# Kernel tuning notes

Measured on AMD Instinct MI355X. Metric: run time of the kernel, lower is better.

The kernel has to match this reference:

```python
import jax, jax.numpy as jnp
import numpy as np

NEG_SLOPE = 0.01  # torch F.leaky_relu default

def _lrelu(x):
    return jax.nn.leaky_relu(x, NEG_SLOPE)

def setup_inputs() -> dict:
    key = jax.random.key(0)
    ks = jax.random.split(key, 24)
    B, N, E = 512, 20000, 640000
    n_enc_1, n_enc_2, n_z = 512, 256, 64
    n_dec_2, n_dec_1, hidden = 256, 512, 256
    p = lambda k, shp, fan: jax.random.normal(k, shp, jnp.float32) * (1.0 / np.sqrt(fan))
    return {
        "data": jax.random.normal(ks[0], (B, N), jnp.float32),
        "noise": jax.random.normal(ks[1], (B, N), jnp.float32),
        "edge_index": jax.random.randint(ks[2], (2, E), 0, N, jnp.int32),
        "w_gcn": jax.random.normal(ks[3], (), jnp.float32),
        "b_gcn": jax.random.normal(ks[4], (), jnp.float32) * 0.1,
        "enc1_w": p(ks[5], (N, n_enc_1), N), "enc1_b": p(ks[6], (n_enc_1,), N),
        "enc2_w": p(ks[7], (n_enc_1, n_enc_2), n_enc_1), "enc2_b": p(ks[8], (n_enc_2,), n_enc_1),
        "enc3_w": p(ks[9], (n_enc_2, n_z), n_enc_2), "enc3_b": p(ks[10], (n_z,), n_enc_2),
        "dec1_w": p(ks[11], (n_z, n_dec_2), n_z), "dec1_b": p(ks[12], (n_dec_2,), n_z),
        "dec2_w": p(ks[13], (n_dec_2, n_dec_1), n_dec_2), "dec2_b": p(ks[14], (n_dec_1,), n_dec_2),
        "dec3_w": p(ks[15], (n_dec_1, N), n_dec_1), "dec3_b": p(ks[16], (N,), n_dec_1),
        "disc1_w": p(ks[17], (n_z, hidden), n_z), "disc1_b": p(ks[18], (hidden,), n_z),
        "disc2_w": p(ks[19], (hidden, hidden), hidden), "disc2_b": p(ks[20], (hidden,), hidden),
        "disc3_w": p(ks[21], (hidden, 1), hidden), "disc3_b": p(ks[22], (1,), hidden),
    }

def _gcn_batched(x, edge_index, w_gcn, b_gcn):
    # x: [B, N] -> GCNConv(1,1, improved=True) applied per row, vectorized.
    B, N = x.shape
    src, dst = edge_index[0], edge_index[1]
    loop = jnp.arange(N, dtype=src.dtype)
    src_a = jnp.concatenate([src, loop])
    dst_a = jnp.concatenate([dst, loop])
    # improved=True: self-loop edge weight 2.0
    ew = jnp.concatenate([jnp.ones(src.shape[0], x.dtype), jnp.full((N,), 2.0, x.dtype)])
    deg = jax.ops.segment_sum(ew, dst_a, num_segments=N)
    dinv = jnp.where(deg > 0, jax.lax.rsqrt(deg), 0.0)
    norm = dinv[src_a] * ew * dinv[dst_a]  # [E+N]
    xl = x * w_gcn                         # lin (1x1 weight, no bias)
    msgs = xl[:, src_a] * norm[None, :]    # [B, E+N]
    agg = jnp.zeros_like(x).at[:, dst_a].add(msgs)
    return agg + b_gcn

def reference(data, noise, edge_index, w_gcn, b_gcn,
              enc1_w, enc1_b, enc2_w, enc2_b, enc3_w, enc3_b,
              dec1_w, dec1_b, dec2_w, dec2_b, dec3_w, dec3_b,
              disc1_w, disc1_b, disc2_w, disc2_b, disc3_w, disc3_b):
    x = data + noise * 0.1
    gcn_out = _lrelu(_gcn_batched(x, edge_index, w_gcn, b_gcn))  # [B, N]
    h1 = _lrelu(gcn_out @ enc1_w + enc1_b)
    h2 = _lrelu(h1 @ enc2_w + enc2_b)
    z = _lrelu(h2 @ enc3_w + enc3_b)
    d1 = _lrelu(z @ dec1_w + dec1_b)
    d2 = _lrelu(d1 @ dec2_w + dec2_b)
    dec_h3 = _lrelu(d2 @ dec3_w + dec3_b)
    g1 = _lrelu(z @ disc1_w + disc1_b)
    g2 = _lrelu(g1 @ disc2_w + disc2_b)
    d = jax.nn.sigmoid(g2 @ disc3_w + disc3_b)
    return (dec_h3, z, d)
```

## Files before the change

### kernel.cpp

```cpp
#include <hip/hip_runtime.h>
#include <hip/hip_bf16.h>


#define LRELU(v) ((v) > 0.f ? (v) : 0.01f * (v))

static constexpr int Bb = 512;
static constexpr int Nn = 20000;
static constexpr int Ee = 640000;
static constexpr int KPAD = 20480;

typedef __attribute__((ext_vector_type(8))) short short8;
typedef __attribute__((ext_vector_type(4))) float f32x4;

__device__ __forceinline__ ushort f2bf(float f) {
  uint u = __builtin_bit_cast(uint, f);
  u = u + 0x7FFFu + ((u >> 16) & 1u);
  return (ushort)(u >> 16);
}
__device__ __forceinline__ float bfLo(uint u) {
  return __builtin_bit_cast(float, u << 16);
}
__device__ __forceinline__ float bfHi(uint u) {
  return __builtin_bit_cast(float, u & 0xffff0000u);
}

__global__ void transpose_xs_k(const float* __restrict__ a, const float* __restrict__ nz,
                               const float* __restrict__ dinv, ushort* __restrict__ xs, int b0) {
  __shared__ ushort tile[64][65];
  int c0 = blockIdx.x * 64;
  int p = blockIdx.y;
  int chunk = p >> 1;
  int sub = (p & 1) * 64;
  int rbase = b0 + p * 64;
  for (int i = threadIdx.x; i < 64 * 64; i += 256) {
    int rr = i >> 6, cc = i & 63;
    int r = rbase + rr, c = c0 + cc;
    ushort v = 0;
    if (c < Nn) {
      size_t idx = (size_t)r * Nn + c;
      v = f2bf(dinv[c] * (a[idx] + 0.1f * nz[idx]));
    }
    tile[rr][cc] = v;
  }
  __syncthreads();
  for (int i = threadIdx.x; i < 64 * 64; i += 256) {
    int cc = i >> 6, rr = i & 63;
    int c = c0 + cc;
    if (c < Nn) xs[(size_t)chunk * Nn * 128 + (size_t)c * 128 + sub + rr] = tile[rr][cc];
  }
}

__global__ void hist_check_k(const int* __restrict__ src, const int* __restrict__ dst, int E,
                             int* __restrict__ cnt, int* __restrict__ flag) {
  int i = blockIdx.x * 256 + threadIdx.x;
  if (i < E) {
    int s = src[i], d = dst[i];
    if ((unsigned)s >= (unsigned)Nn || (unsigned)d >= (unsigned)Nn) {
      atomicExch(flag, 1);
    } else {
      atomicAdd(&cnt[d], 1);
    }
  }
}

__global__ void offs_k(const int* __restrict__ cnt, int* __restrict__ offs,
                       int* __restrict__ cursor, float* __restrict__ dinv,
                       int* __restrict__ bump) {
  int i = blockIdx.x * 256 + threadIdx.x;
  int l = threadIdx.x & 63;
  int v = (i < Nn) ? cnt[i] : 0;
  int x = v;
#pragma unroll
  for (int d = 1; d < 64; d <<= 1) {
    int t = __shfl_up(x, d);
    if (l >= d) x += t;
  }
  int total = __shfl(x, 63);
  int base = 0;
  if (l == 0) base = atomicAdd(bump, total);
  base = __shfl(base, 0);
  int excl = base + x - v;
  if (i < Nn) {
    offs[i] = excl;
    cursor[i] = excl;
    dinv[i] = rsqrtf(2.0f + (float)v);
  }
}

__global__ void scatter_k(const int* __restrict__ src, const int* __restrict__ dst, int E,
                          int* __restrict__ cursor, uint* __restrict__ eOff) {
  int i = blockIdx.x * 256 + threadIdx.x;
  if (i < E) {
    int s = src[i], d = dst[i];
    if ((unsigned)s >= (unsigned)Nn || (unsigned)d >= (unsigned)Nn) return;
    int p = atomicAdd(&cursor[d], 1);
    eOff[p] = (uint)s * 256u;
  }
}

__global__ __launch_bounds__(256) void spmm_chunk_k(
    const ushort* __restrict__ xs, const uint* __restrict__ eOff, const int* __restrict__ offs,
    const int* __restrict__ cnt, const float* __restrict__ dinv, const float* __restrict__ wg,
    const float* __restrict__ bg, ushort* __restrict__ gcnT, int NC) {
  __shared__ uint sIdx[4][64];
  int bid = blockIdx.x;
  int chunk = bid % NC;
  int ngrp = bid / NC;
  int wv = threadIdx.x >> 6, l = threadIdx.x & 63;
  int n = ngrp * 4 + wv;
  int o = offs[n], c = cnt[n];
  const char* base = (const char*)(xs + (size_t)chunk * Nn * 128) + l * 4;
  const uint* ep = eOff + o;
  uint su = *(const uint*)(base + (size_t)n * 256);
  float a00 = 2.0f * bfLo(su), a01 = 2.0f * bfHi(su);
  float a10 = 0.f, a11 = 0.f;

  for (int bi = 0; bi < c; bi += 64) {
    int rem = c - bi;
    if (rem > 64) rem = 64;
    sIdx[wv][l] = (l < rem) ? ep[bi + l] : 0u;
    int i = 0;
    for (; i + 8 <= rem; i += 8) {
      uint u[8];
#pragma unroll
      for (int j = 0; j < 8; ++j) u[j] = *(const uint*)(base + sIdx[wv][i + j]);
#pragma unroll
      for (int j = 0; j < 8; j += 2) {
        a00 += bfLo(u[j]);
        a01 += bfHi(u[j]);
        a10 += bfLo(u[j + 1]);
        a11 += bfHi(u[j + 1]);
      }
    }
    for (; i < rem; ++i) {
      uint u = *(const uint*)(base + sIdx[wv][i]);
      a00 += bfLo(u);
      a01 += bfHi(u);
    }
  }

  float wdn = wg[0] * dinv[n], bb = bg[0];
  float v0 = wdn * (a00 + a10) + bb;
  float v1 = wdn * (a01 + a11) + bb;
  v0 = LRELU(v0);
  v1 = LRELU(v1);
  uint pk = (uint)f2bf(v0) | ((uint)f2bf(v1) << 16);
  *(uint*)&gcnT[(size_t)chunk * KPAD * 128 + (size_t)n * 128 + 2 * l] = pk;
}

template <bool SPLITK>
__global__ __launch_bounds__(256) void mfma_gemm(const ushort* __restrict__ AT, int lda, int pw,
                                                 size_t pstride, const float* __restrict__ B,
                                                 int ldb, int KB, int Nv, int iters,
                                                 float* __restrict__ C, int ldc,
                                                 const float* __restrict__ bias) {
  __shared__ ushort As[32 * 72];
  __shared__ ushort Bs[32 * 72];
  int n0 = blockIdx.x * 64, m0 = blockIdx.y * 64;
  int k0 = blockIdx.z * iters * 32;
  int tid = threadIdx.x;
  int skk = tid >> 3, sx0 = (tid & 7) * 8;
  int l = tid & 63, w = tid >> 6;
  int wr = w >> 1, wc = w & 1;
  int lrow = l & 15, lk8 = (l >> 4) * 8;
  const ushort* Ap = AT + (size_t)(m0 / pw) * pstride + (m0 % pw);
  f32x4 acc[2][2] = {};

  for (int kt = 0; kt < iters; ++kt) {
    int kg = k0 + kt * 32 + skk;
    uint4 av = *(const uint4*)&Ap[(size_t)kg * lda + sx0];
    uint4 bv = {0u, 0u, 0u, 0u};
    if (kg < KB && n0 + sx0 < Nv) {
      const float4* bp = (const float4*)(B + (size_t)kg * ldb + n0 + sx0);
      float4 f0 = bp[0], f1 = bp[1];
      bv.x = (uint)f2bf(f0.x) | ((uint)f2bf(f0.y) << 16);
      bv.y = (uint)f2bf(f0.z) | ((uint)f2bf(f0.w) << 16);
      bv.z = (uint)f2bf(f1.x) | ((uint)f2bf(f1.y) << 16);
      bv.w = (uint)f2bf(f1.z) | ((uint)f2bf(f1.w) << 16);
    }
    __syncthreads();
    *(uint4*)&As[skk * 72 + sx0] = av;
    *(uint4*)&Bs[skk * 72 + sx0] = bv;
    __syncthreads();
    short8 a0, a1, b0, b1;
#pragma unroll
    for (int j = 0; j < 8; ++j) {
      int kr = (lk8 + j) * 72;
      a0[j] = (short)As[kr + wr * 32 + lrow];
      a1[j] = (short)As[kr + wr * 32 + 16 + lrow];
      b0[j] = (short)Bs[kr + wc * 32 + lrow];
      b1[j] = (short)Bs[kr + wc * 32 + 16 + lrow];
    }
    acc[0][0] = __builtin_amdgcn_mfma_f32_16x16x32_bf16(a0, b0, acc[0][0], 0, 0, 0);
    acc[0][1] = __builtin_amdgcn_mfma_f32_16x16x32_bf16(a0, b1, acc[0][1], 0, 0, 0);
    acc[1][0] = __builtin_amdgcn_mfma_f32_16x16x32_bf16(a1, b0, acc[1][0], 0, 0, 0);
    acc[1][1] = __builtin_amdgcn_mfma_f32_16x16x32_bf16(a1, b1, acc[1][1], 0, 0, 0);
  }

#pragma unroll
  for (int fm = 0; fm < 2; ++fm)
#pragma unroll
    for (int fn = 0; fn < 2; ++fn)
#pragma unroll
      for (int r = 0; r < 4; ++r) {
        int row = m0 + wr * 32 + fm * 16 + (l >> 4) * 4 + r;
        int col = n0 + wc * 32 + fn * 16 + lrow;
        if (SPLITK) {
          atomicAdd(&C[(size_t)row * ldc + col], acc[fm][fn][r]);
        } else if (col < Nv) {
          float v = acc[fm][fn][r] + bias[col];
          C[(size_t)row * ldc + col] = LRELU(v);
        }
      }
}

__global__ __launch_bounds__(256) void tail2_k(
    const float* __restrict__ h1, const float* __restrict__ c1, const float* __restrict__ W2,
    const float* __restrict__ c2, const float* __restrict__ W3, const float* __restrict__ c3,
    const float* __restrict__ Wd1, const float* __restrict__ cd1, const float* __restrict__ Wd2,
    const float* __restrict__ cd2, const float* __restrict__ Wg1, const float* __restrict__ cg1,
    const float* __restrict__ Wg2, const float* __restrict__ cg2, const float* __restrict__ Wg3,
    const float* __restrict__ cg3, float* __restrict__ out_z, float* __restrict__ out_d,
    ushort* __restrict__ d2bfT, int BT, int b0) {
  __shared__ float s_h1[512];
  __shared__ float s_h2[256];
  __shared__ float s_z[64];
  __shared__ float s_d1[256];
  __shared__ float s_g1[256];
  __shared__ float s_g2[256];
  __shared__ float s_part[4][256];
  __shared__ float s_red[4];
  int rl = blockIdx.x;
  int rg = b0 + rl;
  int t = threadIdx.x;
  int w = t >> 6, l = t & 63;

  {
    float r0 = h1[(size_t)rl * 512 + t] + c1[t];
    float r1 = h1[(size_t)rl * 512 + t + 256] + c1[t + 256];
    s_h1[t] = LRELU(r0);
    s_h1[t + 256] = LRELU(r1);
  }
  __syncthreads();

  {
    int c4 = l * 4;
    float a0 = 0.f, a1 = 0.f, a2 = 0.f, a3 = 0.f;
#pragma unroll 8
    for (int k = w * 128; k < w * 128 + 128; ++k) {
      float4 wv = *(const float4*)&W2[(size_t)k * 256 + c4];
      float x = s_h1[k];
      a0 += x * wv.x; a1 += x * wv.y; a2 += x * wv.z; a3 += x * wv.w;
    }
    float4 pv = {a0, a1, a2, a3};
    *(float4*)&s_part[w][c4] = pv;
  }
  __syncthreads();
  s_h2[t] = LRELU(s_part[0][t] + s_part[1][t] + s_part[2][t] + s_part[3][t] + c2[t]);
  __syncthreads();

  {
    int c = t >> 2, p = t & 3;
    float a = 0.f;
#pragma unroll 8
    for (int k = p * 64; k < p * 64 + 64; ++k) a += s_h2[k] * W3[(size_t)k * 64 + c];
    s_part[p][c] = a;
  }
  __syncthreads();
  if (t < 64) {
    float v = s_part[0][t] + s_part[1][t] + s_part[2][t] + s_part[3][t] + c3[t];
    v = LRELU(v);
    s_z[t] = v;
    out_z[(size_t)rg * 64 + t] = v;
  }
  __syncthreads();

  {
    float a = 0.f;
#pragma unroll
    for (int k = 0; k < 64; ++k) a += s_z[k] * Wd1[(size_t)k * 256 + t];
    s_d1[t] = LRELU(a + cd1[t]);
  }
  {
    float a = 0.f;
#pragma unroll
    for (int k = 0; k < 64; ++k) a += s_z[k] * Wg1[(size_t)k * 256 + t];
    s_g1[t] = LRELU(a + cg1[t]);
  }
  __syncthreads();

  {
    int g = t & 127, p = t >> 7;
    int c4 = g * 4;
    float a0 = 0.f, a1 = 0.f, a2 = 0.f, a3 = 0.f;
#pragma unroll 8
    for (int k = p * 128; k < p * 128 + 128; ++k) {
      float4 wv = *(const float4*)&Wd2[(size_t)k * 512 + c4];
      float x = s_d1[k];
      a0 += x * wv.x; a1 += x * wv.y; a2 += x * wv.z; a3 += x * wv.w;
    }
    float* sp = &s_part[0][0];
    float4 pv = {a0, a1, a2, a3};
    *(float4*)&sp[p * 512 + c4] = pv;
  }
  __syncthreads();
  {
    const float* sp = &s_part[0][0];
#pragma unroll
    for (int cc = 0; cc < 2; ++cc) {
      int c = t + cc * 256;
      float v = sp[c] + sp[512 + c] + cd2[c];
      v = LRELU(v);
      d2bfT[(size_t)c * BT + rl] = f2bf(v);
    }
  }
  __syncthreads();

  {
    int c4 = l * 4;
    float a0 = 0.f, a1 = 0.f, a2 = 0.f, a3 = 0.f;
#pragma unroll 8
    for (int k = w * 64; k < w * 64 + 64; ++k) {
      float4 wv = *(const float4*)&Wg2[(size_t)k * 256 + c4];
      float x = s_g1[k];
      a0 += x * wv.x; a1 += x * wv.y; a2 += x * wv.z; a3 += x * wv.w;
    }
    float4 pv = {a0, a1, a2, a3};
    *(float4*)&s_part[w][c4] = pv;
  }
  __syncthreads();
  s_g2[t] = LRELU(s_part[0][t] + s_part[1][t] + s_part[2][t] + s_part[3][t] + cg2[t]);
  __syncthreads();

  {
    float p = s_g2[t] * Wg3[t];
#pragma unroll
    for (int o = 32; o > 0; o >>= 1) p += __shfl_down(p, o);
    if ((t & 63) == 0) s_red[t >> 6] = p;
    __syncthreads();
    if (t == 0) {
      float s = s_red[0] + s_red[1] + s_red[2] + s_red[3] + cg3[0];
      out_d[rg] = 1.f / (1.f + __expf(-s));
    }
  }
}

__global__ void sentinel_k(float* out, float val) { out[0] = val; }
__global__ void flag_sentinel_k(float* out, const int* flag) {
  if (*flag != 0) out[0] = 70000.0f;
}

extern "C" void kernel_launch(void* const* d_in, const int* in_sizes, int n_in,
                              void* d_out, int out_size, void* d_ws, size_t ws_size,
                              hipStream_t stream) {
  const float* data = (const float*)d_in[0];
  const float* noise = (const float*)d_in[1];
  const int* edge = (const int*)d_in[2];
  const int* esrc_in = edge;
  const int* edst_in = edge + Ee;
  const float* w_gcn = (const float*)d_in[3];
  const float* b_gcn = (const float*)d_in[4];
  const float* enc1_w = (const float*)d_in[5];
  const float* enc1_b = (const float*)d_in[6];
  const float* enc2_w = (const float*)d_in[7];
  const float* enc2_b = (const float*)d_in[8];
  const float* enc3_w = (const float*)d_in[9];
  const float* enc3_b = (const float*)d_in[10];
  const float* dec1_w = (const float*)d_in[11];
  const float* dec1_b = (const float*)d_in[12];
  const float* dec2_w = (const float*)d_in[13];
  const float* dec2_b = (const float*)d_in[14];
  const float* dec3_w = (const float*)d_in[15];
  const float* dec3_b = (const float*)d_in[16];
  const float* disc1_w = (const float*)d_in[17];
  const float* disc1_b = (const float*)d_in[18];
  const float* disc2_w = (const float*)d_in[19];
  const float* disc2_b = (const float*)d_in[20];
  const float* disc3_w = (const float*)d_in[21];
  const float* disc3_b = (const float*)d_in[22];

  int BT = 128;
  if (ws_size >= 48500000u) BT = 512;
  else if (ws_size >= 24392500u) BT = 256;
  int NC = BT / 128;
  if (NC < 1) NC = 1;

  char* w = (char*)d_ws;
  size_t o = 0;
  auto alloc = [&](size_t bytes) {
    size_t r = o;
    o = (o + bytes + 15) & ~(size_t)15;
    return r;
  };
  ushort* xs = (ushort*)(w + alloc((size_t)Nn * BT * 2));
  ushort* gcnT = (ushort*)(w + alloc((size_t)KPAD * BT * 2));
  float* h1 = (float*)(w + alloc((size_t)BT * 512 * 4));
  ushort* d2bfT = (ushort*)(w + alloc((size_t)512 * BT * 2));
  float* dinv = (float*)(w + alloc(Nn * 4));
  int* cnt = (int*)(w + alloc(Nn * 4));
  int* offs = (int*)(w + alloc(Nn * 4));
  int* cursor = (int*)(w + alloc(Nn * 4));
  uint* eOff = (uint*)(w + alloc(Ee * 4));
  int* flag = (int*)(w + alloc(16));

  float* outp = (float*)d_out;
  float* out_dec = outp;
  float* out_z = outp + (size_t)Bb * Nn;
  float* out_d = out_z + (size_t)Bb * 64;

  static const int expect_sizes[23] = {
      10240000, 10240000, 1280000, 1, 1,
      10240000, 512, 131072, 256, 16384, 64,
      16384, 256, 131072, 512, 10240000, 20000,
      16384, 256, 65536, 256, 256, 1};
  float host_sentinel = 0.f;
  if (n_in != 23) host_sentinel = 50000.f;
  else if (out_size != 10273280) host_sentinel = 80000.f;
  else {
    for (int i = 0; i < 23; ++i)
      if (in_sizes[i] != expect_sizes[i]) { host_sentinel = 100000.f + 1000.f * i; break; }
  }

  hipMemsetAsync(cnt, 0, Nn * sizeof(int), stream);
  hipMemsetAsync(flag, 0, 2 * sizeof(int), stream);
  hist_check_k<<<(Ee + 255) / 256, 256, 0, stream>>>(esrc_in, edst_in, Ee, cnt, flag);
  offs_k<<<(Nn + 255) / 256, 256, 0, stream>>>(cnt, offs, cursor, dinv, flag + 1);
  scatter_k<<<(Ee + 255) / 256, 256, 0, stream>>>(esrc_in, edst_in, Ee, cursor, eOff);
  hipMemsetAsync(gcnT, 0, (size_t)KPAD * BT * 2, stream);

  for (int b0 = 0; b0 < Bb; b0 += BT) {
    {
      dim3 g((Nn + 63) / 64, BT / 64);
      transpose_xs_k<<<g, 256, 0, stream>>>(data, noise, dinv, xs, b0);
    }
    spmm_chunk_k<<<(Nn / 4) * NC, 256, 0, stream>>>(xs, eOff, offs, cnt, dinv, w_gcn, b_gcn,
                                                    gcnT, NC);
    hipMemsetAsync(h1, 0, (size_t)BT * 512 * 4, stream);
    {
      dim3 g(512 / 64, BT / 64, 16);
      mfma_gemm<true><<<g, 256, 0, stream>>>(gcnT, 128, 128, (size_t)KPAD * 128, enc1_w, 512,
                                             Nn, 512, 40, h1, 512, nullptr);
    }
    tail2_k<<<BT, 256, 0, stream>>>(h1, enc1_b, enc2_w, enc2_b, enc3_w, enc3_b, dec1_w, dec1_b,
                                    dec2_w, dec2_b, disc1_w, disc1_b, disc2_w, disc2_b, disc3_w,
                                    disc3_b, out_z, out_d, d2bfT, BT, b0);
    {
      dim3 g((Nn + 63) / 64, BT / 64, 1);
      mfma_gemm<false><<<g, 256, 0, stream>>>(d2bfT, BT, BT, 0, dec3_w, Nn, 512, Nn, 16,
                                              out_dec + (size_t)b0 * Nn, Nn, dec3_b);
    }
  }

  flag_sentinel_k<<<1, 1, 0, stream>>>(out_dec, flag);
  if (host_sentinel != 0.f) sentinel_k<<<1, 1, 0, stream>>>(out_dec, host_sentinel);
}
```

Baseline: 329.9 us.

## Enlarge MFMA GEMM tiles to 128x128 with permuted shared-memory k-rows

Replaces the 64x64 block tile GEMM with a 128x128 tile where each wave computes a 4x4 grid of 16x16 MFMA fragments, raising arithmetic intensity and reducing redundant global loads and fp32->bf16 conversions of the weight matrices. Shared-memory k-rows are stored in a permuted order with a wider stride to change bank access patterns for the fragment reads. The enc1 split-K launch doubles its K splits to keep enough blocks, at the cost of more atomics; register pressure rises with 16 accumulators per wave.

Result: faster. 296.1 us (-10.3%).

```diff
diff --git a/kernel.cpp b/kernel.cpp
--- a/kernel.cpp
+++ b/kernel.cpp
@@ -8,6 +8,7 @@
 static constexpr int Nn = 20000;
 static constexpr int Ee = 640000;
 static constexpr int KPAD = 20480;
+static constexpr int LSTR = 144;
 
 typedef __attribute__((ext_vector_type(8))) short short8;
 typedef __attribute__((ext_vector_type(4))) float f32x4;
@@ -149,66 +150,85 @@
 }
 
 template <bool SPLITK>
-__global__ __launch_bounds__(256) void mfma_gemm(const ushort* __restrict__ AT, int lda, int pw,
-                                                 size_t pstride, const float* __restrict__ B,
-                                                 int ldb, int KB, int Nv, int iters,
-                                                 float* __restrict__ C, int ldc,
-                                                 const float* __restrict__ bias) {
-  __shared__ ushort As[32 * 72];
-  __shared__ ushort Bs[32 * 72];
-  int n0 = blockIdx.x * 64, m0 = blockIdx.y * 64;
+__global__ __launch_bounds__(256) void mfma_gemm2(const ushort* __restrict__ AT, int lda, int pw,
+                                                  size_t pstride, const float* __restrict__ B,
+                                                  int ldb, int KB, int Nv, int iters,
+                                                  float* __restrict__ C, int ldc,
+                                                  const float* __restrict__ bias) {
+  __shared__ ushort As[32 * LSTR];
+  __shared__ ushort Bs[32 * LSTR];
+  int n0 = blockIdx.x * 128, m0 = blockIdx.y * 128;
   int k0 = blockIdx.z * iters * 32;
   int tid = threadIdx.x;
-  int skk = tid >> 3, sx0 = (tid & 7) * 8;
+  int kr = tid >> 4, c8 = (tid & 15) * 8;
   int l = tid & 63, w = tid >> 6;
   int wr = w >> 1, wc = w & 1;
-  int lrow = l & 15, lk8 = (l >> 4) * 8;
+  int lrow = l & 15, lkg = l >> 4;
   const ushort* Ap = AT + (size_t)(m0 / pw) * pstride + (m0 % pw);
-  f32x4 acc[2][2] = {};
+  f32x4 acc[4][4] = {};
 
   for (int kt = 0; kt < iters; ++kt) {
-    int kg = k0 + kt * 32 + skk;
-    uint4 av = *(const uint4*)&Ap[(size_t)kg * lda + sx0];
-    uint4 bv = {0u, 0u, 0u, 0u};
-    if (kg < KB && n0 + sx0 < Nv) {
-      const float4* bp = (const float4*)(B + (size_t)kg * ldb + n0 + sx0);
-      float4 f0 = bp[0], f1 = bp[1];
-      bv.x = (uint)f2bf(f0.x) | ((uint)f2bf(f0.y) << 16);
-      bv.y = (uint)f2bf(f0.z) | ((uint)f2bf(f0.w) << 16);
-      bv.z = (uint)f2bf(f1.x) | ((uint)f2bf(f1.y) << 16);
-      bv.w = (uint)f2bf(f1.z) | ((uint)f2bf(f1.w) << 16);
+    int kg = k0 + kt * 32;
+    uint4 av0 = *(const uint4*)&Ap[(size_t)(kg + kr) * lda + c8];
+    uint4 av1 = *(const uint4*)&Ap[(size_t)(kg + kr + 16) * lda + c8];
+    uint4 bv0 = {0u, 0u, 0u, 0u}, bv1 = {0u, 0u, 0u, 0u};
+    int col = n0 + c8;
+    if (col < Nv) {
+      if (kg + kr < KB) {
+        const float4* bp = (const float4*)(B + (size_t)(kg + kr) * ldb + col);
+        float4 f0 = bp[0], f1 = bp[1];
+        bv0.x = (uint)f2bf(f0.x) | ((uint)f2bf(f0.y) << 16);
+        bv0.y = (uint)f2bf(f0.z) | ((uint)f2bf(f0.w) << 16);
+        bv0.z = (uint)f2bf(f1.x) | ((uint)f2bf(f1.y) << 16);
+        bv0.w = (uint)f2bf(f1.z) | ((uint)f2bf(f1.w) << 16);
+      }
+      if (kg + kr + 16 < KB) {
+        const float4* bp = (const float4*)(B + (size_t)(kg + kr + 16) * ldb + col);
+        float4 f0 = bp[0], f1 = bp[1];
+        bv1.x = (uint)f2bf(f0.x) | ((uint)f2bf(f0.y) << 16);
+        bv1.y = (uint)f2bf(f0.z) | ((uint)f2bf(f0.w) << 16);
+        bv1.z = (uint)f2bf(f1.x) | ((uint)f2bf(f1.y) << 16);
+        bv1.w = (uint)f2bf(f1.z) | ((uint)f2bf(f1.w) << 16);
+      }
     }
     __syncthreads();
-    *(uint4*)&As[skk * 72 + sx0] = av;
-    *(uint4*)&Bs[skk * 72 + sx0] = bv;
+    {
+      int p0 = (kr & 7) * 4 + (kr >> 3);
+      int p1 = ((kr + 16) & 7) * 4 + ((kr + 16) >> 3);
+      *(uint4*)&As[p0 * LSTR + c8] = av0;
+      *(uint4*)&As[p1 * LSTR + c8] = av1;
+      *(uint4*)&Bs[p0 * LSTR + c8] = bv0;
+      *(uint4*)&Bs[p1 * LSTR + c8] = bv1;
+    }
     __syncthreads();
-    short8 a0, a1, b0, b1;
+    short8 a[4], b[4];
 #pragma unroll
     for (int j = 0; j < 8; ++j) {
-      int kr = (lk8 + j) * 72;
-      a0[j] = (short)As[kr + wr * 32 + lrow];
-      a1[j] = (short)As[kr + wr * 32 + 16 + lrow];
-      b0[j] = (short)Bs[kr + wc * 32 + lrow];
-      b1[j] = (short)Bs[kr + wc * 32 + 16 + lrow];
-    }
-    acc[0][0] = __builtin_amdgcn_mfma_f32_16x16x32_bf16(a0, b0, acc[0][0], 0, 0, 0);
-    acc[0][1] = __builtin_amdgcn_mfma_f32_16x16x32_bf16(a0, b1, acc[0][1], 0, 0, 0);
-    acc[1][0] = __builtin_amdgcn_mfma_f32_16x16x32_bf16(a1, b0, acc[1][0], 0, 0, 0);
-    acc[1][1] = __builtin_amdgcn_mfma_f32_16x16x32_bf16(a1, b1, acc[1][1], 0, 0, 0);
-  }
-
-#pragma unroll
-  for (int fm = 0; fm < 2; ++fm)
-#pragma unroll
-    for (int fn = 0; fn < 2; ++fn)
+      int pr = (4 * j + lkg) * LSTR;
+#pragma unroll
+      for (int mi = 0; mi < 4; ++mi) a[mi][j] = (short)As[pr + wr * 64 + mi * 16 + lrow];
+#pragma unroll
+      for (int nj = 0; nj < 4; ++nj) b[nj][j] = (short)Bs[pr + wc * 64 + nj * 16 + lrow];
+    }
+#pragma unroll
+    for (int mi = 0; mi < 4; ++mi)
+#pragma unroll
+      for (int nj = 0; nj < 4; ++nj)
+        acc[mi][nj] = __builtin_amdgcn_mfma_f32_16x16x32_bf16(a[mi], b[nj], acc[mi][nj], 0, 0, 0);
+  }
+
+#pragma unroll
+  for (int mi = 0; mi < 4; ++mi)
+#pragma unroll
+    for (int nj = 0; nj < 4; ++nj)
 #pragma unroll
       for (int r = 0; r < 4; ++r) {
-        int row = m0 + wr * 32 + fm * 16 + (l >> 4) * 4 + r;
-        int col = n0 + wc * 32 + fn * 16 + lrow;
+        int row = m0 + wr * 64 + mi * 16 + lkg * 4 + r;
+        int col = n0 + wc * 64 + nj * 16 + lrow;
         if (SPLITK) {
-          atomicAdd(&C[(size_t)row * ldc + col], acc[fm][fn][r]);
+          atomicAdd(&C[(size_t)row * ldc + col], acc[mi][nj][r]);
         } else if (col < Nv) {
-          float v = acc[fm][fn][r] + bias[col];
+          float v = acc[mi][nj][r] + bias[col];
           C[(size_t)row * ldc + col] = LRELU(v);
         }
       }
@@ -437,17 +457,17 @@
                                                     gcnT, NC);
     hipMemsetAsync(h1, 0, (size_t)BT * 512 * 4, stream);
     {
-      dim3 g(512 / 64, BT / 64, 16);
-      mfma_gemm<true><<<g, 256, 0, stream>>>(gcnT, 128, 128, (size_t)KPAD * 128, enc1_w, 512,
-                                             Nn, 512, 40, h1, 512, nullptr);
+      dim3 g(512 / 128, BT / 128, 32);
+      mfma_gemm2<true><<<g, 256, 0, stream>>>(gcnT, 128, 128, (size_t)KPAD * 128, enc1_w, 512,
+                                              Nn, 512, 20, h1, 512, nullptr);
     }
     tail2_k<<<BT, 256, 0, stream>>>(h1, enc1_b, enc2_w, enc2_b, enc3_w, enc3_b, dec1_w, dec1_b,
                                     dec2_w, dec2_b, disc1_w, disc1_b, disc2_w, disc2_b, disc3_w,
                                     disc3_b, out_z, out_d, d2bfT, BT, b0);
     {
-      dim3 g((Nn + 63) / 64, BT / 64, 1);
-      mfma_gemm<false><<<g, 256, 0, stream>>>(d2bfT, BT, BT, 0, dec3_w, Nn, 512, Nn, 16,
-                                              out_dec + (size_t)b0 * Nn, Nn, dec3_b);
+      dim3 g((Nn + 127) / 128, BT / 128, 1);
+      mfma_gemm2<false><<<g, 256, 0, stream>>>(d2bfT, BT, BT, 0, dec3_w, Nn, 512, Nn, 16,
+                                               out_dec + (size_t)b0 * Nn, Nn, dec3_b);
     }
   }
 
```
